# Kernel optimization log

Measured on AMD Instinct MI355X. Metric: run time of the kernel, lower is better.

Reference implementation:

```python
import jax, jax.numpy as jnp
import numpy as np

B, N_PER_GRAPH, DEG = 4, 50000, 32
NUM_RELS, NUM_BASES, N_LAYERS = 8, 4, 2
E_PER = N_PER_GRAPH * DEG
N_TOTAL = B * N_PER_GRAPH
E_TOTAL = B * E_PER


def setup_inputs() -> dict:
    key = jax.random.key(0)
    ks = jax.random.split(key, 10)
    # Block-structured edges: each graph's edges stay within its node block (dgl.batch semantics)
    src_b = jax.random.randint(ks[0], (B, E_PER), 0, N_PER_GRAPH)
    dst_b = jax.random.randint(ks[1], (B, E_PER), 0, N_PER_GRAPH)
    off = (jnp.arange(B) * N_PER_GRAPH)[:, None]
    src = (src_b + off).reshape(-1).astype(jnp.int64)
    dst = (dst_b + off).reshape(-1).astype(jnp.int64)
    edge_type = jax.random.randint(ks[2], (E_TOTAL,), 0, NUM_RELS).astype(jnp.int64)
    norm = jax.random.uniform(ks[3], (E_TOTAL, 1), dtype=jnp.float32)
    feat1 = jax.random.normal(ks[4], (N_TOTAL, 1), dtype=jnp.float32)
    feat2 = jax.random.normal(ks[5], (N_TOTAL, 1), dtype=jnp.float32)
    # RGCN basis-decomposition params per layer (in=out=h_dim=1)
    bases = jax.random.normal(ks[6], (N_LAYERS, NUM_BASES, 1, 1), dtype=jnp.float32) * 0.1
    w_comp = jax.random.normal(ks[7], (N_LAYERS, NUM_RELS, NUM_BASES), dtype=jnp.float32) * 0.1
    biases = jnp.zeros((N_LAYERS, 1), dtype=jnp.float32)  # DGL RelGraphConv bias (out_dim=1)
    W_lin = jax.random.normal(ks[8], (1024, N_PER_GRAPH), dtype=jnp.float32) / np.float32(np.sqrt(N_PER_GRAPH))
    b_lin = jnp.zeros((1024,), dtype=jnp.float32)
    return dict(feat1=feat1, feat2=feat2, src=src, dst=dst, edge_type=edge_type,
                norm=norm, num_nodes=N_PER_GRAPH, bases=bases, w_comp=w_comp,
                biases=biases, W_lin=W_lin, b_lin=b_lin)


def _forward_each(feat, src, dst, edge_type, norm, bases, w_comp, biases, W_lin, b_lin, num_nodes):
    n_total = feat.shape[0]
    n_layers = w_comp.shape[0]
    initial = feat
    x = feat
    for l in range(n_layers):
        # basis decomposition: per-relation (1x1) weight -> scalar per relation
        weight = (w_comp[l] @ bases[l].reshape(NUM_BASES, 1))  # (num_rels, 1)
        msg = x[src] * weight[edge_type] * norm               # (E, 1) gather + edge-wise transform
        agg = jax.ops.segment_sum(msg, dst, num_segments=n_total)  # scatter-sum per node
        h = agg + biases[l]
        if l < n_layers - 1:
            h = jax.nn.relu(h)
        x = h + initial  # residual add (x += initial)
    x = x.reshape(-1, num_nodes)          # (B, num_nodes) since h_dim == 1
    return x @ W_lin.T + b_lin            # (B, 1024)


def reference(feat1, feat2, src, dst, edge_type, norm, num_nodes, bases, w_comp, biases, W_lin, b_lin):
    x1 = _forward_each(feat1, src, dst, edge_type, norm, bases, w_comp, biases, W_lin, b_lin, num_nodes)
    x2 = _forward_each(feat2, src, dst, edge_type, norm, bases, w_comp, biases, W_lin, b_lin, num_nodes)
    x = jnp.sum(x1 * x2, axis=1, keepdims=True)  # (B, 1)
    return jax.nn.sigmoid(x)
```

## Files before the change

kernel.cpp:

```cpp
#include <hip/hip_runtime.h>
#include <hip/hip_bf16.h>
#include <math.h>

#define BB 4
#define N_PER 50000
#define DEG 32
#define NUM_RELS 8
#define NUM_BASES 4
#define N_LAYERS 2
#define E_PER (N_PER * DEG)
#define E_TOTAL (BB * E_PER)
#define N_TOTAL (BB * N_PER)
#define OUT_F 1024

#define RANGES 4
#define RANGE_SZ (N_PER / RANGES)
#define SUBS 16
#define EDGES_PER_BLOCK (E_PER / SUBS)
#define GROUPS_PER_BLOCK (EDGES_PER_BLOCK / 4)
#define PARTIAL_STRIDE (2 * RANGE_SZ)
#define NBLOCKS (BB * RANGES * SUBS)


__global__ __launch_bounds__(256) void init_kernel(
    const float* __restrict__ feat1, const float* __restrict__ feat2,
    const float* __restrict__ bases, const float* __restrict__ w_comp,
    float* __restrict__ ws) {
  int tid = blockIdx.x * blockDim.x + threadIdx.x;
  if (blockIdx.x == 0) {
    if (threadIdx.x < 16) {
      int l = threadIdx.x >> 3, r = threadIdx.x & 7;
      float s = 0.f;
#pragma unroll
      for (int b = 0; b < NUM_BASES; ++b)
        s += w_comp[l * NUM_RELS * NUM_BASES + r * NUM_BASES + b] *
             bases[l * NUM_BASES + b];
      ws[l * 8 + r] = s;
    } else if (threadIdx.x < 20) {
      ws[16 + (threadIdx.x - 16)] = 0.f;
    }
  }
  float* x1 = ws + 32;
  float* x2 = x1 + N_TOTAL;
  for (int i = tid; i < N_TOTAL; i += gridDim.x * blockDim.x) {
    x1[i] = feat1[i];
    x2[i] = feat2[i];
  }
}

__global__ __launch_bounds__(1024) void edge_bin_kernel(
    const int* __restrict__ src, const int* __restrict__ dst,
    const int* __restrict__ et, const float* __restrict__ norm,
    const float* __restrict__ relw, int layer,
    const float* __restrict__ x1, const float* __restrict__ x2,
    float* __restrict__ partials) {
  __shared__ float w[NUM_RELS];
  __shared__ float bin1[RANGE_SZ];
  __shared__ float bin2[RANGE_SZ];
  int bid = blockIdx.x;
  int sub = bid & (SUBS - 1);
  int br = bid >> 4;
  int b = br >> 2, r = br & 3;
  if (threadIdx.x < NUM_RELS) w[threadIdx.x] = relw[layer * 8 + threadIdx.x];
  for (int i = threadIdx.x; i < RANGE_SZ; i += blockDim.x) {
    bin1[i] = 0.f;
    bin2[i] = 0.f;
  }
  __syncthreads();

  int base = b * E_PER + sub * EDGES_PER_BLOCK;
  int node_lo = b * N_PER + r * RANGE_SZ;
  for (int g = threadIdx.x; g < GROUPS_PER_BLOCK; g += blockDim.x) {
    int e = base + g * 4;
    int4 s4 = *(const int4*)(src + e);
    int4 d4 = *(const int4*)(dst + e);
    int4 t4 = *(const int4*)(et + e);
    float4 n4 = *(const float4*)(norm + e);
    {
      int lr = d4.x - node_lo;
      if (lr >= 0 && lr < RANGE_SZ) {
        float c = w[t4.x] * n4.x;
        atomicAdd(&bin1[lr], x1[s4.x] * c);
        atomicAdd(&bin2[lr], x2[s4.x] * c);
      }
    }
    {
      int lr = d4.y - node_lo;
      if (lr >= 0 && lr < RANGE_SZ) {
        float c = w[t4.y] * n4.y;
        atomicAdd(&bin1[lr], x1[s4.y] * c);
        atomicAdd(&bin2[lr], x2[s4.y] * c);
      }
    }
    {
      int lr = d4.z - node_lo;
      if (lr >= 0 && lr < RANGE_SZ) {
        float c = w[t4.z] * n4.z;
        atomicAdd(&bin1[lr], x1[s4.z] * c);
        atomicAdd(&bin2[lr], x2[s4.z] * c);
      }
    }
    {
      int lr = d4.w - node_lo;
      if (lr >= 0 && lr < RANGE_SZ) {
        float c = w[t4.w] * n4.w;
        atomicAdd(&bin1[lr], x1[s4.w] * c);
        atomicAdd(&bin2[lr], x2[s4.w] * c);
      }
    }
  }
  __syncthreads();

  float* outp = partials + (size_t)bid * PARTIAL_STRIDE;
  for (int i = threadIdx.x; i < RANGE_SZ; i += blockDim.x) {
    outp[i] = bin1[i];
    outp[RANGE_SZ + i] = bin2[i];
  }
}

__global__ __launch_bounds__(256) void merge_node_kernel(
    const float* __restrict__ partials,
    const float* __restrict__ feat1, const float* __restrict__ feat2,
    const float* __restrict__ biases, int layer,
    float* __restrict__ x1, float* __restrict__ x2) {
  int i = blockIdx.x * 256 + threadIdx.x;
  if (i >= N_TOTAL) return;
  int b = i / N_PER;
  int local = i - b * N_PER;
  int r = local / RANGE_SZ;
  int lidx = local - r * RANGE_SZ;
  int blk0 = (b * RANGES + r) * SUBS;
  float s1 = 0.f, s2 = 0.f;
#pragma unroll
  for (int s = 0; s < SUBS; ++s) {
    const float* p = partials + (size_t)(blk0 + s) * PARTIAL_STRIDE;
    s1 += p[lidx];
    s2 += p[RANGE_SZ + lidx];
  }
  float bias = biases[layer];
  float h1 = s1 + bias, h2 = s2 + bias;
  if (layer < N_LAYERS - 1) {
    h1 = fmaxf(h1, 0.f);
    h2 = fmaxf(h2, 0.f);
  }
  x1[i] = h1 + feat1[i];
  x2[i] = h2 + feat2[i];
}

__global__ __launch_bounds__(256) void gemv_kernel(
    const float* __restrict__ W, const float* __restrict__ b_lin,
    const float* __restrict__ x1, const float* __restrict__ x2,
    float* __restrict__ acc) {
  int j = blockIdx.x;
  const float* wr = W + (size_t)j * N_PER;
  float a1[4] = {0.f, 0.f, 0.f, 0.f};
  float a2[4] = {0.f, 0.f, 0.f, 0.f};
  for (int k = threadIdx.x * 4; k <= N_PER - 4; k += 256 * 4) {
    float4 wv = *(const float4*)(wr + k);
#pragma unroll
    for (int i = 0; i < 4; ++i) {
      float4 v1 = *(const float4*)(x1 + i * N_PER + k);
      float4 v2 = *(const float4*)(x2 + i * N_PER + k);
      a1[i] += wv.x * v1.x + wv.y * v1.y + wv.z * v1.z + wv.w * v1.w;
      a2[i] += wv.x * v2.x + wv.y * v2.y + wv.z * v2.z + wv.w * v2.w;
    }
  }
#pragma unroll
  for (int off = 32; off > 0; off >>= 1) {
#pragma unroll
    for (int i = 0; i < 4; ++i) {
      a1[i] += __shfl_down(a1[i], off);
      a2[i] += __shfl_down(a2[i], off);
    }
  }
  __shared__ float red[4][8];
  int wave = threadIdx.x >> 6, lane = threadIdx.x & 63;
  if (lane == 0) {
#pragma unroll
    for (int i = 0; i < 4; ++i) {
      red[wave][i] = a1[i];
      red[wave][4 + i] = a2[i];
    }
  }
  __syncthreads();
  if (threadIdx.x == 0) {
    float bl = b_lin[j];
#pragma unroll
    for (int i = 0; i < 4; ++i) {
      float y1 = red[0][i] + red[1][i] + red[2][i] + red[3][i] + bl;
      float y2 = red[0][4 + i] + red[1][4 + i] + red[2][4 + i] + red[3][4 + i] + bl;
      atomicAdd(&acc[i], y1 * y2);
    }
  }
}

__global__ void sigmoid_kernel(const float* __restrict__ acc,
                               float* __restrict__ out) {
  int i = threadIdx.x;
  if (i < BB) out[i] = 1.f / (1.f + expf(-acc[i]));
}

extern "C" void kernel_launch(void* const* d_in, const int* in_sizes, int n_in,
                              void* d_out, int out_size, void* d_ws, size_t ws_size,
                              hipStream_t stream) {
  const float* feat1 = (const float*)d_in[0];
  const float* feat2 = (const float*)d_in[1];
  const int* src = (const int*)d_in[2];
  const int* dst = (const int*)d_in[3];
  const int* et = (const int*)d_in[4];
  const float* norm = (const float*)d_in[5];
  const float* bases = (const float*)d_in[7];
  const float* w_comp = (const float*)d_in[8];
  const float* biases = (const float*)d_in[9];
  const float* W_lin = (const float*)d_in[10];
  const float* b_lin = (const float*)d_in[11];
  float* out = (float*)d_out;

  float* ws = (float*)d_ws;
  float* relw = ws;
  float* acc = ws + 16;
  float* x1 = ws + 32;
  float* x2 = x1 + N_TOTAL;
  float* partials = x2 + N_TOTAL;

  int nblk = (N_TOTAL + 255) / 256;
  init_kernel<<<nblk, 256, 0, stream>>>(feat1, feat2, bases, w_comp, ws);

  for (int l = 0; l < N_LAYERS; ++l) {
    edge_bin_kernel<<<NBLOCKS, 1024, 0, stream>>>(src, dst, et, norm, relw, l,
                                                  x1, x2, partials);
    merge_node_kernel<<<nblk, 256, 0, stream>>>(partials, feat1, feat2, biases,
                                                l, x1, x2);
  }

  gemv_kernel<<<OUT_F, 256, 0, stream>>>(W_lin, b_lin, x1, x2, acc);
  sigmoid_kernel<<<1, 64, 0, stream>>>(acc, out);
}
```

Measured before the change: 621.7 us.

## Block GEMV over 8 output rows with K-split and fused final reduction

Each GEMV block now handles 8 output rows over one tenth of the K dimension. The x1/x2 vectors loaded once per K step are reused across all 8 W rows, instead of being reloaded for every output row. Per-block partials go to workspace, and a single 1024-thread kernel sums them, adds the bias, forms the per-graph dot products and applies the sigmoid. This removes the global atomics and the separate sigmoid launch. In exchange there are 64 accumulators per thread, which raises register pressure, plus an extra pass over the partials.

```diff
diff --git a/kernel.cpp b/kernel.cpp
--- a/kernel.cpp
+++ b/kernel.cpp
@@ -21,24 +21,26 @@
 #define PARTIAL_STRIDE (2 * RANGE_SZ)
 #define NBLOCKS (BB * RANGES * SUBS)
 
+#define GR 8
+#define GKSPLIT 10
+#define GKCHUNK (N_PER / GKSPLIT)
+#define GROWBLKS (OUT_F / GR)
+#define GEMV_BLOCKS (GROWBLKS * GKSPLIT)
+
 
 __global__ __launch_bounds__(256) void init_kernel(
     const float* __restrict__ feat1, const float* __restrict__ feat2,
     const float* __restrict__ bases, const float* __restrict__ w_comp,
     float* __restrict__ ws) {
   int tid = blockIdx.x * blockDim.x + threadIdx.x;
-  if (blockIdx.x == 0) {
-    if (threadIdx.x < 16) {
-      int l = threadIdx.x >> 3, r = threadIdx.x & 7;
-      float s = 0.f;
-#pragma unroll
-      for (int b = 0; b < NUM_BASES; ++b)
-        s += w_comp[l * NUM_RELS * NUM_BASES + r * NUM_BASES + b] *
-             bases[l * NUM_BASES + b];
-      ws[l * 8 + r] = s;
-    } else if (threadIdx.x < 20) {
-      ws[16 + (threadIdx.x - 16)] = 0.f;
-    }
+  if (blockIdx.x == 0 && threadIdx.x < 16) {
+    int l = threadIdx.x >> 3, r = threadIdx.x & 7;
+    float s = 0.f;
+#pragma unroll
+    for (int b = 0; b < NUM_BASES; ++b)
+      s += w_comp[l * NUM_RELS * NUM_BASES + r * NUM_BASES + b] *
+           bases[l * NUM_BASES + b];
+    ws[l * 8 + r] = s;
   }
   float* x1 = ws + 32;
   float* x2 = x1 + N_TOTAL;
@@ -147,57 +149,101 @@
   x2[i] = h2 + feat2[i];
 }
 
-__global__ __launch_bounds__(256) void gemv_kernel(
-    const float* __restrict__ W, const float* __restrict__ b_lin,
+__global__ __launch_bounds__(256) void gemv_part_kernel(
+    const float* __restrict__ W,
     const float* __restrict__ x1, const float* __restrict__ x2,
-    float* __restrict__ acc) {
-  int j = blockIdx.x;
-  const float* wr = W + (size_t)j * N_PER;
-  float a1[4] = {0.f, 0.f, 0.f, 0.f};
-  float a2[4] = {0.f, 0.f, 0.f, 0.f};
-  for (int k = threadIdx.x * 4; k <= N_PER - 4; k += 256 * 4) {
-    float4 wv = *(const float4*)(wr + k);
+    float* __restrict__ gpart) {
+  int bid = blockIdx.x;
+  int rb = bid & (GROWBLKS - 1);
+  int ks = bid >> 7;
+  int j0 = rb * GR;
+  int k0 = ks * GKCHUNK;
+
+  float acc[GR][8];
+#pragma unroll
+  for (int r = 0; r < GR; ++r)
+#pragma unroll
+    for (int g = 0; g < 8; ++g) acc[r][g] = 0.f;
+
+  for (int k = k0 + threadIdx.x * 4; k < k0 + GKCHUNK; k += 256 * 4) {
+    float4 xv[8];
 #pragma unroll
     for (int i = 0; i < 4; ++i) {
-      float4 v1 = *(const float4*)(x1 + i * N_PER + k);
-      float4 v2 = *(const float4*)(x2 + i * N_PER + k);
-      a1[i] += wv.x * v1.x + wv.y * v1.y + wv.z * v1.z + wv.w * v1.w;
-      a2[i] += wv.x * v2.x + wv.y * v2.y + wv.z * v2.z + wv.w * v2.w;
-    }
-  }
-#pragma unroll
-  for (int off = 32; off > 0; off >>= 1) {
-#pragma unroll
-    for (int i = 0; i < 4; ++i) {
-      a1[i] += __shfl_down(a1[i], off);
-      a2[i] += __shfl_down(a2[i], off);
-    }
-  }
-  __shared__ float red[4][8];
+      xv[2 * i] = *(const float4*)(x1 + i * N_PER + k);
+      xv[2 * i + 1] = *(const float4*)(x2 + i * N_PER + k);
+    }
+#pragma unroll
+    for (int r = 0; r < GR; ++r) {
+      float4 wv = *(const float4*)(W + (size_t)(j0 + r) * N_PER + k);
+#pragma unroll
+      for (int g = 0; g < 8; ++g) {
+        acc[r][g] += wv.x * xv[g].x + wv.y * xv[g].y +
+                     wv.z * xv[g].z + wv.w * xv[g].w;
+      }
+    }
+  }
+
+#pragma unroll
+  for (int off = 32; off > 0; off >>= 1)
+#pragma unroll
+    for (int r = 0; r < GR; ++r)
+#pragma unroll
+      for (int g = 0; g < 8; ++g) acc[r][g] += __shfl_down(acc[r][g], off);
+
+  __shared__ float red[4][GR * 8];
   int wave = threadIdx.x >> 6, lane = threadIdx.x & 63;
   if (lane == 0) {
 #pragma unroll
-    for (int i = 0; i < 4; ++i) {
-      red[wave][i] = a1[i];
-      red[wave][4 + i] = a2[i];
-    }
-  }
-  __syncthreads();
-  if (threadIdx.x == 0) {
-    float bl = b_lin[j];
-#pragma unroll
-    for (int i = 0; i < 4; ++i) {
-      float y1 = red[0][i] + red[1][i] + red[2][i] + red[3][i] + bl;
-      float y2 = red[0][4 + i] + red[1][4 + i] + red[2][4 + i] + red[3][4 + i] + bl;
-      atomicAdd(&acc[i], y1 * y2);
-    }
-  }
-}
-
-__global__ void sigmoid_kernel(const float* __restrict__ acc,
-                               float* __restrict__ out) {
-  int i = threadIdx.x;
-  if (i < BB) out[i] = 1.f / (1.f + expf(-acc[i]));
+    for (int r = 0; r < GR; ++r)
+#pragma unroll
+      for (int g = 0; g < 8; ++g) red[wave][r * 8 + g] = acc[r][g];
+  }
+  __syncthreads();
+  if (threadIdx.x < GR * 8) {
+    float s = red[0][threadIdx.x] + red[1][threadIdx.x] +
+              red[2][threadIdx.x] + red[3][threadIdx.x];
+    gpart[(size_t)bid * (GR * 8) + threadIdx.x] = s;
+  }
+}
+
+__global__ __launch_bounds__(1024) void gemv_reduce_kernel(
+    const float* __restrict__ gpart, const float* __restrict__ b_lin,
+    float* __restrict__ out) {
+  int j = threadIdx.x;
+  int rb = j >> 3, rr = j & 7;
+  float y[8];
+#pragma unroll
+  for (int g = 0; g < 8; ++g) y[g] = 0.f;
+#pragma unroll
+  for (int ks = 0; ks < GKSPLIT; ++ks) {
+    const float* p = gpart + (size_t)(ks * GROWBLKS + rb) * (GR * 8) + rr * 8;
+#pragma unroll
+    for (int g = 0; g < 8; ++g) y[g] += p[g];
+  }
+  float bl = b_lin[j];
+  float prod[4];
+#pragma unroll
+  for (int i = 0; i < 4; ++i)
+    prod[i] = (y[2 * i] + bl) * (y[2 * i + 1] + bl);
+
+#pragma unroll
+  for (int off = 32; off > 0; off >>= 1)
+#pragma unroll
+    for (int i = 0; i < 4; ++i) prod[i] += __shfl_down(prod[i], off);
+
+  __shared__ float red[16][4];
+  int wave = threadIdx.x >> 6, lane = threadIdx.x & 63;
+  if (lane == 0) {
+#pragma unroll
+    for (int i = 0; i < 4; ++i) red[wave][i] = prod[i];
+  }
+  __syncthreads();
+  if (threadIdx.x < 4) {
+    float s = 0.f;
+#pragma unroll
+    for (int wv = 0; wv < 16; ++wv) s += red[wv][threadIdx.x];
+    out[threadIdx.x] = 1.f / (1.f + expf(-s));
+  }
 }
 
 extern "C" void kernel_launch(void* const* d_in, const int* in_sizes, int n_in,
@@ -218,7 +264,6 @@
 
   float* ws = (float*)d_ws;
   float* relw = ws;
-  float* acc = ws + 16;
   float* x1 = ws + 32;
   float* x2 = x1 + N_TOTAL;
   float* partials = x2 + N_TOTAL;
@@ -233,6 +278,7 @@
                                                 l, x1, x2);
   }
 
-  gemv_kernel<<<OUT_F, 256, 0, stream>>>(W_lin, b_lin, x1, x2, acc);
-  sigmoid_kernel<<<1, 64, 0, stream>>>(acc, out);
-}
+  float* gpart = partials;
+  gemv_part_kernel<<<GEMV_BLOCKS, 256, 0, stream>>>(W_lin, x1, x2, gpart);
+  gemv_reduce_kernel<<<1, 1024, 0, stream>>>(gpart, b_lin, out);
+}
```

Measured after the change: 554.9 us. 1.12x faster.
